# Kernel tuning notes

Hardware: AMD Instinct MI355X
Metric: run time of the kernel (lower is better)

## Reference

```python
import jax, jax.numpy as jnp
import numpy as np
from jax import lax

N_LAYERS = 3


def setup_inputs() -> dict:
    key = jax.random.key(0)
    ks = jax.random.split(key, 10)
    B, E, H, O, L = 64, 1024, 1024, 64, N_LAYERS
    s = 1.0 / np.sqrt(H)  # keep gate pre-activations in a sane range
    return {
        "batch_enc": jax.random.normal(ks[0], (B, E), jnp.float32),
        "h0": jax.random.normal(ks[1], (L, B, H), jnp.float32),
        "c0": jax.random.normal(ks[2], (L, B, H), jnp.float32),
        "W_ih": jax.random.normal(ks[3], (L, 4 * H, E), jnp.float32) * s,
        "W_hh": jax.random.normal(ks[4], (L, 4 * H, H), jnp.float32) * s,
        "b_ih": jax.random.normal(ks[5], (L, 4 * H), jnp.float32) * s,
        "b_hh": jax.random.normal(ks[6], (L, 4 * H), jnp.float32) * s,
        "W_lin": jax.random.normal(ks[7], (O, H), jnp.float32) * s,
        "b_lin": jax.random.normal(ks[8], (O,), jnp.float32) * s,
        "out_len": 1024,
    }


def _lstm_layer(x_seq, h0, c0, W_ih, W_hh, b_ih, b_hh):
    # x_seq: [T, B, in]. Precompute input projection once (input is the same
    # every step in this decoder, but this form is general and still fused).
    x_proj = jnp.einsum('tbi,gi->tbg', x_seq, W_ih) + (b_ih + b_hh)  # [T,B,4H]

    def step(carry, xp):
        h, c = carry
        gates = xp + h @ W_hh.T  # [B,4H]
        i, f, g, o = jnp.split(gates, 4, axis=-1)  # PyTorch gate order i,f,g,o
        i = jax.nn.sigmoid(i)
        f = jax.nn.sigmoid(f)
        g = jnp.tanh(g)
        o = jax.nn.sigmoid(o)
        c = f * c + i * g
        h = o * jnp.tanh(c)
        return (h, c), h

    _, ys = lax.scan(step, (h0, c0), x_proj)
    return ys  # [T, B, H]


def reference(batch_enc, h0, c0, W_ih, W_hh, b_ih, b_hh, W_lin, b_lin, out_len):
    B = batch_enc.shape[0]
    T = int(out_len)
    # decoder input: encoding repeated across all timesteps (time-major)
    x = jnp.broadcast_to(batch_enc[None, :, :], (T, B, batch_enc.shape[1]))
    for l in range(N_LAYERS):
        x = _lstm_layer(x, h0[l], c0[l], W_ih[l], W_hh[l], b_ih[l], b_hh[l])
    out = x @ W_lin.T + b_lin  # [T, B, out_elem_size]
    return jnp.transpose(out, (1, 0, 2))  # [B, T, out_elem_size]
```

## Files before the change

kernel.cpp:

```cpp
#include <hip/hip_runtime.h>
#include <hip/hip_bf16.h>
#include <hip/hip_fp16.h>


typedef _Float16 v8h __attribute__((ext_vector_type(8)));
typedef _Float16 v4h __attribute__((ext_vector_type(4)));
typedef float v4f __attribute__((ext_vector_type(4)));

#define NSTEPS 1029
#define AGG 192

__device__ inline void store16_wt(void* p, v8h v) {
    asm volatile("global_store_dwordx4 %0, %1, off sc0 sc1" :: "v"(p), "v"(v) : "memory");
}
__device__ inline void store8_wt(void* p, unsigned long long v) {
    asm volatile("global_store_dwordx2 %0, %1, off sc0 sc1" :: "v"(p), "v"(v) : "memory");
}

__global__ void cvt4_kernel(const float* __restrict__ s, _Float16* __restrict__ d, int n4) {
    int i = blockIdx.x * blockDim.x + threadIdx.x;
    int stride = gridDim.x * blockDim.x;
    for (; i < n4; i += stride) {
        v4f v = ((const v4f*)s)[i];
        v4h o;
        o[0] = (_Float16)v[0]; o[1] = (_Float16)v[1];
        o[2] = (_Float16)v[2]; o[3] = (_Float16)v[3];
        ((v4h*)d)[i] = o;
    }
}

__global__ void hinit_kernel(const float* __restrict__ h0, _Float16* __restrict__ hbuf) {
    int i = blockIdx.x * 256 + threadIdx.x;
    int l = i >> 16, rem = i & 65535;
    hbuf[(l * 2 + 1) * 65536 + rem] = (_Float16)h0[i];
}

__global__ void zflags_kernel(unsigned* f) { int i = threadIdx.x; if (i < 260) f[i] = 0u; }

__global__ __launch_bounds__(256) void xp0_kernel(
    const _Float16* __restrict__ enc16, const _Float16* __restrict__ Wih,
    const float* __restrict__ b_ih, const float* __restrict__ b_hh,
    float* __restrict__ xp0) {
    __shared__ float red[16384];
    const int tid = threadIdx.x, bx = blockIdx.x;
    const int ln = tid & 63, w = tid >> 6, lm = ln & 15, q = ln >> 4;
    v4f acc[4][4] = {};
    for (int kb = 0; kb < 8; ++kb) {
        int kk = (w + 4 * kb) * 32 + q * 8;
        v8h af[4], bf[4];
#pragma unroll
        for (int mt = 0; mt < 4; ++mt) af[mt] = *(const v8h*)(enc16 + (mt * 16 + lm) * 1024 + kk);
#pragma unroll
        for (int nt = 0; nt < 4; ++nt) bf[nt] = *(const v8h*)(Wih + (bx * 64 + nt * 16 + lm) * 1024 + kk);
#pragma unroll
        for (int mt = 0; mt < 4; ++mt)
#pragma unroll
            for (int nt = 0; nt < 4; ++nt)
                acc[mt][nt] = __builtin_amdgcn_mfma_f32_16x16x32_f16(af[mt], bf[nt], acc[mt][nt], 0, 0, 0);
    }
#pragma unroll
    for (int mt = 0; mt < 4; ++mt) if (mt != w)
#pragma unroll
        for (int nt = 0; nt < 4; ++nt)
            *(v4f*)&red[((w * 16 + mt * 4 + nt) * 64 + ln) * 4] = acc[mt][nt];
    __syncthreads();
#pragma unroll
    for (int ww = 0; ww < 4; ++ww) if (ww != w)
#pragma unroll
        for (int nt = 0; nt < 4; ++nt)
            acc[w][nt] += *(const v4f*)&red[((ww * 16 + w * 4 + nt) * 64 + ln) * 4];
#pragma unroll
    for (int nt = 0; nt < 4; ++nt) {
        int g = bx * 64 + nt * 16 + lm;
        float bb = b_ih[g] + b_hh[g];
#pragma unroll
        for (int r = 0; r < 4; ++r) {
            int b = w * 16 + q * 4 + r;
            xp0[b * 4096 + g] = acc[w][nt][r] + bb;
        }
    }
}

__global__ __launch_bounds__(256, 1) void lstm_persist(
    const _Float16* __restrict__ Wih16,
    const _Float16* __restrict__ Whh16,
    const _Float16* __restrict__ Wlin16,
    const float* __restrict__ xp0,
    const float* __restrict__ b_ih,
    const float* __restrict__ b_hh,
    const float* __restrict__ c0,
    const float* __restrict__ blin,
    _Float16* __restrict__ hbuf,
    _Float16* __restrict__ pbuf,
    float* __restrict__ out,
    unsigned* __restrict__ flags,
    unsigned* __restrict__ go)
{
    __shared__ v4f red[2][12][64];
    __shared__ _Float16 ldsW[16384];
    const int b = blockIdx.x, tid = threadIdx.x;
    const int ln = tid & 63, w = tid >> 6, lm = ln & 15, q = ln >> 4;
    const int bt0 = w * 16 + q * 4;

    const bool isFin = b < 192;
    const int l = b >> 6, hs = b & 63;
    int sidR[5], sidL; bool hasL;
    if (isFin) {
        hasL = true;
        sidR[0] = sidR[1] = sidR[2] = sidR[3] = -1; sidR[4] = -2;
        int s4;
        if (b < 64) s4 = b;
        else if (b < 128) s4 = 256 + (b - 64);
        else if (b < 132) s4 = 512 + (b - 128);
        else s4 = 64 + (b - 132);
        sidL = s4;
    } else {
        int j = b - 192;
        int i0 = (j < 60) ? 5 * j : 300 + 6 * (j - 60);
        hasL = (j >= 60);
#pragma unroll
        for (int u = 0; u < 5; ++u) { int id = i0 + u; sidR[u] = (id < 132) ? 124 + id : 188 + id; }
        sidL = hasL ? 188 + i0 + 5 : -2;
    }

    const _Float16* wb[6]; int asel[6], lo[6], hi[6], pcol[6], pl[6]; bool prj[6], act[6];
#pragma unroll
    for (int m = 0; m < 6; ++m) {
        int sd = (m < 5) ? sidR[m] : sidL;
        act[m] = (isFin && m < 4) || sd >= 0;
        prj[m] = false; pl[m] = 0; pcol[m] = 0;
        if (isFin && m < 4) {
            wb[m] = Whh16 + l * 4194304 + (m * 1024 + hs * 16) * 1024;
            asel[m] = l; lo[m] = 1 << 30; hi[m] = 0;
        } else if (sd >= 512) {
            wb[m] = Wlin16 + (sd - 512) * 16384;
            asel[m] = 2; lo[m] = 5; hi[m] = 1029; prj[m] = true; pcol[m] = (sd - 512) * 16;
        } else if (sd >= 256) {
            wb[m] = Wih16 + 2 * 4194304 + (sd - 256) * 16384;
            asel[m] = 1; lo[m] = 3; hi[m] = 1027; pl[m] = 1; pcol[m] = (sd - 256) * 16;
        } else if (sd >= 0) {
            wb[m] = Wih16 + 4194304 + sd * 16384;
            asel[m] = 0; lo[m] = 1; hi[m] = 1025; pl[m] = 0; pcol[m] = sd * 16;
        } else {
            wb[m] = wb[0]; asel[m] = 0; lo[m] = 1 << 30; hi[m] = 0;
        }
    }
    const int aselP = asel[0];
    int aselS = aselP; bool useS[6]; bool anyS = false;
#pragma unroll
    for (int m = 0; m < 6; ++m) {
        if (!act[m]) asel[m] = aselP;
        useS[m] = (asel[m] != aselP);
        if (useS[m]) { aselS = asel[m]; anyS = true; }
    }

    const int kofs = w * 256 + q * 8;
    v8h wf[5][8];
#pragma unroll
    for (int m = 0; m < 5; ++m) {
        const _Float16* wr = wb[m] + lm * 1024 + kofs;
#pragma unroll
        for (int kb = 0; kb < 8; ++kb) wf[m][kb] = *(const v8h*)(wr + kb * 32);
    }
    if (hasL) {
        const _Float16* wr = wb[5];
        for (int it = tid; it < 2048; it += 256)
            *(v8h*)&ldsW[it * 8] = *(const v8h*)(wr + it * 8);
    }
    __syncthreads();

    float c4[4] = {0.f, 0.f, 0.f, 0.f};
    float xpr[4][4]; float bsum[4] = {0.f, 0.f, 0.f, 0.f};
    if (isFin) {
#pragma unroll
        for (int r = 0; r < 4; ++r)
            c4[r] = c0[(l * 64 + bt0 + r) * 1024 + hs * 16 + lm];
        if (l == 0) {
#pragma unroll
            for (int u = 0; u < 4; ++u)
#pragma unroll
                for (int r = 0; r < 4; ++r)
                    xpr[u][r] = xp0[(bt0 + r) * 4096 + u * 1024 + hs * 16 + lm];
        } else {
#pragma unroll
            for (int u = 0; u < 4; ++u) {
                int g = u * 1024 + hs * 16 + lm;
                bsum[u] = b_ih[l * 4096 + g] + b_hh[l * 4096 + g];
            }
        }
    }
    float blv = 0.f;
    if (hasL && prj[5]) blv = blin[pcol[5] + lm];

    for (int s = 0; s < NSTEPS; ++s) {
        const unsigned su = (unsigned)(s + 1);
        const int rslot = (s + 1) & 1, wslot = s & 1;
        const int tF = s - 2 * l;
        const bool finValid = isFin && ((unsigned)tF < 1024u);

        float pv[4][4];
        if (isFin && l >= 1 && finValid) {
            const _Float16* pr = pbuf + ((l - 1) * 2 + (s & 1)) * 262144;
#pragma unroll
            for (int u = 0; u < 4; ++u) {
                v4h t4 = *(const v4h*)&pr[(u * 1024 + hs * 16 + lm) * 64 + bt0];
#pragma unroll
                for (int r = 0; r < 4; ++r) pv[u][r] = (float)t4[r];
            }
        }

        v4f accR[5][4], accL[4];
        const v4f vz = {0.f, 0.f, 0.f, 0.f};
#pragma unroll
        for (int m = 0; m < 5; ++m)
#pragma unroll
            for (int j = 0; j < 4; ++j) accR[m][j] = vz;
#pragma unroll
        for (int j = 0; j < 4; ++j) accL[j] = vz;

        const _Float16* hPb = hbuf + (aselP * 2 + rslot) * 65536 + kofs;
        const _Float16* hSb = hbuf + (aselS * 2 + rslot) * 65536 + kofs;
#pragma unroll
        for (int kb = 0; kb < 8; ++kb) {
            v8h fp[4], fs[4];
#pragma unroll
            for (int j = 0; j < 4; ++j) {
                int mt = (w + j) & 3;
                fp[j] = *(const v8h*)(hPb + kb * 32 + (mt * 16 + lm) * 1024);
            }
            if (anyS) {
#pragma unroll
                for (int j = 0; j < 4; ++j) {
                    int mt = (w + j) & 3;
                    fs[j] = *(const v8h*)(hSb + kb * 32 + (mt * 16 + lm) * 1024);
                }
            } else {
#pragma unroll
                for (int j = 0; j < 4; ++j) fs[j] = fp[j];
            }
            v8h wl;
            if (hasL) wl = *(const v8h*)&ldsW[lm * 1024 + kofs + kb * 32];
#pragma unroll
            for (int m = 0; m < 5; ++m) {
                if (!act[m]) continue;
#pragma unroll
                for (int j = 0; j < 4; ++j)
                    accR[m][j] = __builtin_amdgcn_mfma_f32_16x16x32_f16(useS[m] ? fs[j] : fp[j], wf[m][kb], accR[m][j], 0, 0, 0);
            }
            if (hasL)
#pragma unroll
                for (int j = 0; j < 4; ++j)
                    accL[j] = __builtin_amdgcn_mfma_f32_16x16x32_f16(useS[5] ? fs[j] : fp[j], wl, accL[j], 0, 0, 0);
        }

#pragma unroll
        for (int p = 0; p < 3; ++p) {
            __syncthreads();
            {   int m = 2 * p;
                if (act[m])
#pragma unroll
                    for (int j = 1; j < 4; ++j) {
                        int dst = (w + j) & 3;
                        red[0][dst * 3 + w - (w > dst ? 1 : 0)][ln] = accR[m][j];
                    }
            }
            if (p < 2) {
                int m = 2 * p + 1;
                if (act[m])
#pragma unroll
                    for (int j = 1; j < 4; ++j) {
                        int dst = (w + j) & 3;
                        red[1][dst * 3 + w - (w > dst ? 1 : 0)][ln] = accR[m][j];
                    }
            } else if (hasL) {
#pragma unroll
                for (int j = 1; j < 4; ++j) {
                    int dst = (w + j) & 3;
                    red[1][dst * 3 + w - (w > dst ? 1 : 0)][ln] = accL[j];
                }
            }
            __syncthreads();
            {   int m = 2 * p;
                if (act[m])
#pragma unroll
                    for (int sj = 1; sj < 4; ++sj) {
                        int src = (w + sj) & 3;
                        accR[m][0] += red[0][w * 3 + src - (src > w ? 1 : 0)][ln];
                    }
            }
            if (p < 2) {
                int m = 2 * p + 1;
                if (act[m])
#pragma unroll
                    for (int sj = 1; sj < 4; ++sj) {
                        int src = (w + sj) & 3;
                        accR[m][0] += red[1][w * 3 + src - (src > w ? 1 : 0)][ln];
                    }
            } else if (hasL) {
#pragma unroll
                for (int sj = 1; sj < 4; ++sj) {
                    int src = (w + sj) & 3;
                    accL[0] += red[1][w * 3 + src - (src > w ? 1 : 0)][ln];
                }
            }
        }

        if (isFin) {
            float hv[4];
            if (finValid) {
#pragma unroll
                for (int r = 0; r < 4; ++r) {
                    float gi = accR[0][0][r], gf = accR[1][0][r], gg = accR[2][0][r], go_ = accR[3][0][r];
                    if (l == 0) { gi += xpr[0][r]; gf += xpr[1][r]; gg += xpr[2][r]; go_ += xpr[3][r]; }
                    else { gi += bsum[0] + pv[0][r]; gf += bsum[1] + pv[1][r];
                           gg += bsum[2] + pv[2][r]; go_ += bsum[3] + pv[3][r]; }
                    gi = 1.f / (1.f + __expf(-gi));
                    gf = 1.f / (1.f + __expf(-gf));
                    go_ = 1.f / (1.f + __expf(-go_));
                    gg = 2.f / (1.f + __expf(-2.f * gg)) - 1.f;
                    float c = gf * c4[r] + gi * gg;
                    c4[r] = c;
                    float th = 2.f / (1.f + __expf(-2.f * c)) - 1.f;
                    hv[r] = go_ * th;
                }
            }
            __syncthreads();
            _Float16* hsh = (_Float16*)red;
            if (finValid)
#pragma unroll
                for (int r = 0; r < 4; ++r) hsh[(bt0 + r) * 16 + lm] = (_Float16)hv[r];
            __syncthreads();
            if (finValid && tid < 128) {
                int row = tid >> 1, half = tid & 1;
                v8h hv8 = *(v8h*)&hsh[row * 16 + half * 8];
                store16_wt(hbuf + (l * 2 + wslot) * 65536 + row * 1024 + hs * 16 + half * 8, hv8);
            }
        }

#pragma unroll
        for (int m = 0; m < 6; ++m) {
            if (isFin && m < 4) continue;
            if (!act[m]) continue;
            if (s < lo[m] || s >= hi[m]) continue;
            v4f a = (m < 5) ? accR[m][0] : accL[0];
            if (prj[m]) {
                int t = s - 5;
#pragma unroll
                for (int r = 0; r < 4; ++r)
                    out[((bt0 + r) * 1024 + t) * 64 + pcol[m] + lm] = a[r] + blv;
            } else {
                union { unsigned long long u64; _Float16 h4[4]; } pk;
#pragma unroll
                for (int r = 0; r < 4; ++r) pk.h4[r] = (_Float16)a[r];
                store8_wt(pbuf + (pl[m] * 2 + ((s + 1) & 1)) * 262144 + (pcol[m] + lm) * 64 + bt0, pk.u64);
            }
        }

        asm volatile("s_waitcnt vmcnt(0)" ::: "memory");
        __syncthreads();
        if (tid == 0)
            __hip_atomic_store(&flags[b], su, __ATOMIC_RELAXED, __HIP_MEMORY_SCOPE_AGENT);
        if (b == AGG) {
            unsigned v;
            do {
                v = __hip_atomic_load(&flags[tid], __ATOMIC_RELAXED, __HIP_MEMORY_SCOPE_AGENT);
            } while (v < su);
            __syncthreads();
            if (tid == 0)
                __hip_atomic_store(go, su, __ATOMIC_RELAXED, __HIP_MEMORY_SCOPE_AGENT);
        }
        if (tid == 0) {
            while (__hip_atomic_load(go, __ATOMIC_RELAXED, __HIP_MEMORY_SCOPE_AGENT) < su)
                __builtin_amdgcn_s_sleep(1);
            (void)__hip_atomic_load(go, __ATOMIC_ACQUIRE, __HIP_MEMORY_SCOPE_AGENT);
        }
        __syncthreads();
    }
}

extern "C" void kernel_launch(void* const* d_in, const int* in_sizes, int n_in,
                              void* d_out, int out_size, void* d_ws, size_t ws_size,
                              hipStream_t stream) {
    const float* enc   = (const float*)d_in[0];
    const float* h0    = (const float*)d_in[1];
    const float* c0    = (const float*)d_in[2];
    const float* W_ih  = (const float*)d_in[3];
    const float* W_hh  = (const float*)d_in[4];
    const float* b_ih  = (const float*)d_in[5];
    const float* b_hh  = (const float*)d_in[6];
    const float* W_lin = (const float*)d_in[7];
    const float* b_lin = (const float*)d_in[8];
    float* out = (float*)d_out;
    char* ws = (char*)d_ws;

    _Float16* Wih16  = (_Float16*)(ws);
    _Float16* Whh16  = (_Float16*)(ws + 25165824);
    _Float16* Wlin16 = (_Float16*)(ws + 50331648);
    _Float16* enc16  = (_Float16*)(ws + 50462720);
    float*    xp0    = (float*)   (ws + 50593792);
    _Float16* hbuf   = (_Float16*)(ws + 51642368);
    _Float16* pbuf   = (_Float16*)(ws + 52428800);
    unsigned* flags  = (unsigned*)(ws + 50462720);
    unsigned* go     = flags + 256;

    cvt4_kernel<<<2048, 256, 0, stream>>>(W_ih, Wih16, 3145728);
    cvt4_kernel<<<2048, 256, 0, stream>>>(W_hh, Whh16, 3145728);
    cvt4_kernel<<<64, 256, 0, stream>>>(W_lin, Wlin16, 16384);
    cvt4_kernel<<<64, 256, 0, stream>>>(enc, enc16, 16384);
    hinit_kernel<<<768, 256, 0, stream>>>(h0, hbuf);
    xp0_kernel<<<64, 256, 0, stream>>>(enc16, Wih16, b_ih, b_hh, xp0);
    zflags_kernel<<<1, 512, 0, stream>>>(flags);

    lstm_persist<<<256, 256, 0, stream>>>(Wih16, Whh16, Wlin16, xp0, b_ih, b_hh,
                                          c0, b_lin, hbuf, pbuf, out, flags, go);
}
```

Baseline: 14.74 ms.

## Replace aggregator grid barrier with all-block flag polling and single-pass LDS reduction

The grid-wide barrier no longer routes through one aggregator block that sets a go flag. Every block now polls all 256 flags directly with vectorized sc1 loads across one wavefront, which removes one hop of cross-block latency per step. Stores switch from sc0 sc1 write-through to sc1 only. The cross-wave reduction becomes a single pass with one barrier instead of three rounds of two barriers, using a larger LDS buffer. The LDS weight tile is padded to cut bank conflicts. In exchange, all blocks now poll the flag lines at once, adding memory traffic and contention.

New measurement: 19.10 ms. 29.6% more time.

```diff
diff --git a/kernel.cpp b/kernel.cpp
--- a/kernel.cpp
+++ b/kernel.cpp
@@ -6,15 +6,21 @@
 typedef _Float16 v8h __attribute__((ext_vector_type(8)));
 typedef _Float16 v4h __attribute__((ext_vector_type(4)));
 typedef float v4f __attribute__((ext_vector_type(4)));
+typedef unsigned uint4v __attribute__((ext_vector_type(4)));
 
 #define NSTEPS 1029
-#define AGG 192
-
-__device__ inline void store16_wt(void* p, v8h v) {
-    asm volatile("global_store_dwordx4 %0, %1, off sc0 sc1" :: "v"(p), "v"(v) : "memory");
-}
-__device__ inline void store8_wt(void* p, unsigned long long v) {
-    asm volatile("global_store_dwordx2 %0, %1, off sc0 sc1" :: "v"(p), "v"(v) : "memory");
+
+__device__ inline void store16_dev(void* p, v8h v) {
+    asm volatile("global_store_dwordx4 %0, %1, off sc1" :: "v"(p), "v"(v) : "memory");
+}
+__device__ inline void store8_dev(void* p, unsigned long long v) {
+    asm volatile("global_store_dwordx2 %0, %1, off sc1" :: "v"(p), "v"(v) : "memory");
+}
+__device__ inline uint4v load16_dev(const void* p) {
+    uint4v v;
+    asm volatile("global_load_dwordx4 %0, %1, off sc1\n\ts_waitcnt vmcnt(0)"
+                 : "=v"(v) : "v"(p) : "memory");
+    return v;
 }
 
 __global__ void cvt4_kernel(const float* __restrict__ s, _Float16* __restrict__ d, int n4) {
@@ -93,11 +99,11 @@
     _Float16* __restrict__ hbuf,
     _Float16* __restrict__ pbuf,
     float* __restrict__ out,
-    unsigned* __restrict__ flags,
-    unsigned* __restrict__ go)
+    unsigned* __restrict__ flags)
 {
-    __shared__ v4f red[2][12][64];
-    __shared__ _Float16 ldsW[16384];
+    __shared__ v4f red[4608];
+    __shared__ _Float16 ldsW[16512];
+    __shared__ _Float16 hsh[1024];
     const int b = blockIdx.x, tid = threadIdx.x;
     const int ln = tid & 63, w = tid >> 6, lm = ln & 15, q = ln >> 4;
     const int bt0 = w * 16 + q * 4;
@@ -165,7 +171,7 @@
     if (hasL) {
         const _Float16* wr = wb[5];
         for (int it = tid; it < 2048; it += 256)
-            *(v8h*)&ldsW[it * 8] = *(const v8h*)(wr + it * 8);
+            *(v8h*)&ldsW[(it >> 7) * 1032 + ((it & 127) << 3)] = *(const v8h*)(wr + it * 8);
     }
     __syncthreads();
 
@@ -239,7 +245,7 @@
                 for (int j = 0; j < 4; ++j) fs[j] = fp[j];
             }
             v8h wl;
-            if (hasL) wl = *(const v8h*)&ldsW[lm * 1024 + kofs + kb * 32];
+            if (hasL) wl = *(const v8h*)&ldsW[lm * 1032 + kofs + kb * 32];
 #pragma unroll
             for (int m = 0; m < 5; ++m) {
                 if (!act[m]) continue;
@@ -254,54 +260,25 @@
         }
 
 #pragma unroll
-        for (int p = 0; p < 3; ++p) {
-            __syncthreads();
-            {   int m = 2 * p;
-                if (act[m])
-#pragma unroll
-                    for (int j = 1; j < 4; ++j) {
-                        int dst = (w + j) & 3;
-                        red[0][dst * 3 + w - (w > dst ? 1 : 0)][ln] = accR[m][j];
-                    }
-            }
-            if (p < 2) {
-                int m = 2 * p + 1;
-                if (act[m])
-#pragma unroll
-                    for (int j = 1; j < 4; ++j) {
-                        int dst = (w + j) & 3;
-                        red[1][dst * 3 + w - (w > dst ? 1 : 0)][ln] = accR[m][j];
-                    }
-            } else if (hasL) {
-#pragma unroll
-                for (int j = 1; j < 4; ++j) {
-                    int dst = (w + j) & 3;
-                    red[1][dst * 3 + w - (w > dst ? 1 : 0)][ln] = accL[j];
-                }
-            }
-            __syncthreads();
-            {   int m = 2 * p;
-                if (act[m])
-#pragma unroll
-                    for (int sj = 1; sj < 4; ++sj) {
-                        int src = (w + sj) & 3;
-                        accR[m][0] += red[0][w * 3 + src - (src > w ? 1 : 0)][ln];
-                    }
-            }
-            if (p < 2) {
-                int m = 2 * p + 1;
-                if (act[m])
-#pragma unroll
-                    for (int sj = 1; sj < 4; ++sj) {
-                        int src = (w + sj) & 3;
-                        accR[m][0] += red[1][w * 3 + src - (src > w ? 1 : 0)][ln];
-                    }
-            } else if (hasL) {
-#pragma unroll
-                for (int sj = 1; sj < 4; ++sj) {
-                    int src = (w + sj) & 3;
-                    accL[0] += red[1][w * 3 + src - (src > w ? 1 : 0)][ln];
-                }
+        for (int m = 0; m < 6; ++m) {
+            bool a = (m < 5) ? act[m] : hasL;
+            if (!a) continue;
+#pragma unroll
+            for (int j = 1; j < 4; ++j) {
+                int dst = (w + j) & 3;
+                int si = w - (w > dst ? 1 : 0);
+                red[((m * 4 + dst) * 3 + si) * 64 + ln] = (m < 5) ? accR[m][j] : accL[j];
+            }
+        }
+        __syncthreads();
+#pragma unroll
+        for (int m = 0; m < 6; ++m) {
+            bool a = (m < 5) ? act[m] : hasL;
+            if (!a) continue;
+#pragma unroll
+            for (int si = 0; si < 3; ++si) {
+                v4f t = red[((m * 4 + w) * 3 + si) * 64 + ln];
+                if (m < 5) accR[m][0] += t; else accL[0] += t;
             }
         }
 
@@ -323,17 +300,14 @@
                     float th = 2.f / (1.f + __expf(-2.f * c)) - 1.f;
                     hv[r] = go_ * th;
                 }
-            }
-            __syncthreads();
-            _Float16* hsh = (_Float16*)red;
-            if (finValid)
 #pragma unroll
                 for (int r = 0; r < 4; ++r) hsh[(bt0 + r) * 16 + lm] = (_Float16)hv[r];
+            }
             __syncthreads();
             if (finValid && tid < 128) {
                 int row = tid >> 1, half = tid & 1;
                 v8h hv8 = *(v8h*)&hsh[row * 16 + half * 8];
-                store16_wt(hbuf + (l * 2 + wslot) * 65536 + row * 1024 + hs * 16 + half * 8, hv8);
+                store16_dev(hbuf + (l * 2 + wslot) * 65536 + row * 1024 + hs * 16 + half * 8, hv8);
             }
         }
 
@@ -352,7 +326,7 @@
                 union { unsigned long long u64; _Float16 h4[4]; } pk;
 #pragma unroll
                 for (int r = 0; r < 4; ++r) pk.h4[r] = (_Float16)a[r];
-                store8_wt(pbuf + (pl[m] * 2 + ((s + 1) & 1)) * 262144 + (pcol[m] + lm) * 64 + bt0, pk.u64);
+                store8_dev(pbuf + (pl[m] * 2 + ((s + 1) & 1)) * 262144 + (pcol[m] + lm) * 64 + bt0, pk.u64);
             }
         }
 
@@ -360,20 +334,17 @@
         __syncthreads();
         if (tid == 0)
             __hip_atomic_store(&flags[b], su, __ATOMIC_RELAXED, __HIP_MEMORY_SCOPE_AGENT);
-        if (b == AGG) {
-            unsigned v;
-            do {
-                v = __hip_atomic_load(&flags[tid], __ATOMIC_RELAXED, __HIP_MEMORY_SCOPE_AGENT);
-            } while (v < su);
-            __syncthreads();
-            if (tid == 0)
-                __hip_atomic_store(go, su, __ATOMIC_RELAXED, __HIP_MEMORY_SCOPE_AGENT);
-        }
-        if (tid == 0) {
-            while (__hip_atomic_load(go, __ATOMIC_RELAXED, __HIP_MEMORY_SCOPE_AGENT) < su)
+        if (tid < 64) {
+            const unsigned* fp4 = flags + tid * 4;
+            for (;;) {
+                uint4v v = load16_dev(fp4);
+                bool ok = v[0] >= su && v[1] >= su && v[2] >= su && v[3] >= su;
+                if (__ballot(ok) == ~0ull) break;
                 __builtin_amdgcn_s_sleep(1);
-            (void)__hip_atomic_load(go, __ATOMIC_ACQUIRE, __HIP_MEMORY_SCOPE_AGENT);
-        }
+            }
+        }
+        if (tid == 0)
+            (void)__hip_atomic_load(&flags[0], __ATOMIC_ACQUIRE, __HIP_MEMORY_SCOPE_AGENT);
         __syncthreads();
     }
 }
@@ -401,7 +372,6 @@
     _Float16* hbuf   = (_Float16*)(ws + 51642368);
     _Float16* pbuf   = (_Float16*)(ws + 52428800);
     unsigned* flags  = (unsigned*)(ws + 50462720);
-    unsigned* go     = flags + 256;
 
     cvt4_kernel<<<2048, 256, 0, stream>>>(W_ih, Wih16, 3145728);
     cvt4_kernel<<<2048, 256, 0, stream>>>(W_hh, Whh16, 3145728);
@@ -412,5 +382,5 @@
     zflags_kernel<<<1, 512, 0, stream>>>(flags);
 
     lstm_persist<<<256, 256, 0, stream>>>(Wih16, Whh16, Wlin16, xp0, b_ih, b_hh,
-                                          c0, b_lin, hbuf, pbuf, out, flags, go);
-}
+                                          c0, b_lin, hbuf, pbuf, out, flags);
+}
```
